# Optimization experiments

Measured on AMD Instinct MI355X. Metric: run time of the kernel, lower is better.

The kernel has to match this reference:

```python
import jax, jax.numpy as jnp
import numpy as np

B, T, K = 64, 4096, 48  # batch, seq_len, n_tags


def setup_inputs() -> dict:
    key = jax.random.key(0)
    k1, k2, k3 = jax.random.split(key, 3)
    labels = jax.random.randint(k1, (B, T), 0, K)
    y_true = jax.nn.one_hot(labels, K, dtype=jnp.float32)  # one-hot targets, per dense_loss docstring
    y_pred = jax.random.normal(k2, (B, T, K), dtype=jnp.float32)  # emission scores
    trans = jax.random.normal(k3, (K, K), dtype=jnp.float32) * 0.1  # transition matrix (glorot-ish scale)
    return {"y_true": y_true, "y_pred": y_pred, "trans": trans}


def reference(y_true, y_pred, trans):
    # mask: positions where all emission scores > -1e6 (padding marker)
    mask = jnp.all(y_pred > -1e6, axis=2, keepdims=True).astype(y_pred.dtype)  # (B,T,1)
    y_true = y_true * mask
    y_pred = y_pred * mask

    # target_score: per-label emission score + transition score of the true path
    point_score = jnp.einsum('bni,bni->b', y_true, y_pred)
    trans_score = jnp.einsum('bni,ij,bnj->b', y_true[:, :-1], trans, y_true[:, 1:])
    target = point_score + trans_score  # (B,)

    # log_norm_step recurrence (CRF forward algorithm), fused as a single scan
    init = y_pred[:, 0]  # (B,K)
    xs = jnp.swapaxes(y_pred[:, 1:], 0, 1)  # (T-1,B,K)
    ms = jnp.swapaxes(mask[:, 1:], 0, 1)    # (T-1,B,1)

    def step(s, xm):
        x, m = xm
        # logsumexp over previous-tag axis: s (B,K_prev) + trans (K_prev,K_cur)
        new = jax.scipy.special.logsumexp(s[:, :, None] + trans[None, :, :], axis=1) + x
        s = m * new + (1.0 - m) * s
        return s, None

    s_final, _ = jax.lax.scan(step, init, (xs, ms))
    log_norm = jax.scipy.special.logsumexp(s_final, axis=1)  # (B,)

    # dense_loss returns log_norm - target_score (negative log-likelihood per example)
    return log_norm - target
```

## Files before the change

### kernel.cpp

```cpp
#include <hip/hip_runtime.h>

#define BB 64
#define TT 4096
#define KK 48
#define UST 56
#define PST 56
#define WS_LS_OFF 16384
#define WS_U_OFF 32768
#define SEGBYTES 6144

typedef __bf16 bf16_t;
typedef bf16_t bf16x8 __attribute__((ext_vector_type(8)));
typedef float f32x4 __attribute__((ext_vector_type(4)));
typedef float f32x16 __attribute__((ext_vector_type(16)));

__device__ __forceinline__ float fexp(float x) {
    return __builtin_amdgcn_exp2f(x * 1.4426950408889634f);
}
__device__ __forceinline__ float flog2(float x) { return __builtin_amdgcn_logf(x); }
__device__ __forceinline__ float rdlanef(float v, int l) {
    return __int_as_float(__builtin_amdgcn_readlane(__float_as_int(v), l));
}
__device__ __forceinline__ unsigned int bf16bits(float f) {
    return (unsigned int)__builtin_bit_cast(unsigned short, (bf16_t)f);
}
__device__ __forceinline__ float bf2f(bf16_t h) {
    return __uint_as_float(((unsigned int)__builtin_bit_cast(unsigned short, h)) << 16);
}
__device__ __forceinline__ unsigned int pktrunc(float lo, float hi) {
    return __builtin_amdgcn_perm(__float_as_uint(hi), __float_as_uint(lo), 0x07060302u);
}

__global__ __launch_bounds__(256) void fused_kernel(
    const float* __restrict__ y_true, const float* __restrict__ y_pred,
    const float* __restrict__ trans, float* __restrict__ ws_target,
    int* __restrict__ ws_ls, bf16_t* __restrict__ ws_u, int nseg) {
    const int s = blockIdx.x, b = blockIdx.y;
    const int seglen = TT / nseg;
    const int nch = seglen / 64;
    const int tid = threadIdx.x;
    const int w = tid >> 6;
    const int lane = tid & 63;
    const int q = lane >> 4;
    const int n = lane & 15;
    const int ncol = 16 * w + n;

    __shared__ __align__(16) float4 exf[64 * 13];
    __shared__ __align__(16) bf16_t Ubuf[48 * UST + 16];
    __shared__ unsigned long long pb;
    __shared__ int lsb[4];

    bf16x8 afrag[3][2];
    if (w < 3) {
#pragma unroll
        for (int mt = 0; mt < 3; mt++) {
#pragma unroll
            for (int ks = 0; ks < 2; ks++) {
                bf16x8 f;
#pragma unroll
                for (int j = 0; j < 8; j++) {
                    int k = 32 * ks + 8 * q + j;
                    float v = (k < KK) ? fexp(trans[k * KK + 16 * mt + n]) : 0.0f;
                    f[j] = (bf16_t)v;
                }
                afrag[mt][ks] = f;
            }
        }
    }

    {
        uint4* p = (uint4*)Ubuf;
        for (int i = tid; i < (48 * UST + 16) / 8; i += 256) p[i] = make_uint4(0, 0, 0, 0);
    }
    __syncthreads();
    if (tid < KK) Ubuf[tid * UST + tid] = (bf16_t)1.0f;

    const bf16_t* bptr0 = &Ubuf[ncol * UST + 8 * q];
    const bf16_t* bptr1 = &Ubuf[ncol * UST + 32 + 8 * q];
    bf16_t* wp0 = &Ubuf[ncol * UST + 0 + 4 * q];
    bf16_t* wp1 = &Ubuf[ncol * UST + 16 + 4 * q];
    bf16_t* wp2 = &Ubuf[ncol * UST + 32 + 4 * q];

    f32x4 z4 = {0.0f, 0.0f, 0.0f, 0.0f};
    int ls = 0;
    int cnt = 0;
    float sc_acc = 0.0f;

    for (int ch = 0; ch < nch; ch++) {
        __syncthreads();
        if (w == 3) {
            const int t0c = s * seglen + ch * 64;
            const size_t rowbase = ((size_t)b * TT + t0c + lane) * KK;
            const float4* yp4 = (const float4*)(y_pred + rowbase);
            const float4* yt4 = (const float4*)(y_true + rowbase);
            float dot = 0.0f, labf = 0.0f, pmin = 1e30f;
            float4* exrow = &exf[lane * 13];
#pragma unroll 4
            for (int g = 0; g < 12; g++) {
                float4 p = yp4[g];
                float4 a = yt4[g];
                dot = fmaf(a.x, p.x, fmaf(a.y, p.y, fmaf(a.z, p.z, fmaf(a.w, p.w, dot))));
                float e0 = (float)(4 * g);
                labf = fmaf(a.x, e0, fmaf(a.y, e0 + 1.0f, fmaf(a.z, e0 + 2.0f, fmaf(a.w, e0 + 3.0f, labf))));
                pmin = fminf(pmin, fminf(fminf(p.x, p.y), fminf(p.z, p.w)));
                exrow[g] = make_float4(fexp(p.x), fexp(p.y), fexp(p.z), fexp(p.w));
            }
            bool mt_ok = pmin > -1e6f;
            unsigned long long bal = __ballot(mt_ok);
            if (lane == 0) pb = bal;

            float labB = 0.0f, pmB = 1e30f;
            const bool hasB = (t0c + 64 < TT);
            if (hasB && lane < 12) {
                const size_t bdbase = ((size_t)b * TT + t0c + 64) * KK;
                float4 a = ((const float4*)(y_true + bdbase))[lane];
                float4 p = ((const float4*)(y_pred + bdbase))[lane];
                float e0 = (float)(4 * lane);
                labB = fmaf(a.x, e0, fmaf(a.y, e0 + 1.0f, fmaf(a.z, e0 + 2.0f, a.w * (e0 + 3.0f))));
                pmB = fminf(fminf(p.x, p.y), fminf(p.z, p.w));
            }
#pragma unroll
            for (int off = 1; off < 16; off <<= 1) {
                labB += __shfl_xor(labB, off);
                pmB = fminf(pmB, __shfl_xor(pmB, off));
            }
            int labB_i = (int)(rdlanef(labB, 0) + 0.5f);
            float mB = (hasB && rdlanef(pmB, 0) > -1e6f) ? 1.0f : 0.0f;

            int labt = (int)(labf + 0.5f);
            float mft = mt_ok ? 1.0f : 0.0f;
            int lnx = __shfl(labt, (lane + 1) & 63);
            float mnx = __shfl(mft, (lane + 1) & 63);
            if (lane == 63) { lnx = labB_i; mnx = mB; }
            sc_acc += mft * dot + mft * mnx * trans[labt * KK + lnx];
        }
        __syncthreads();
        if (w < 3) {
            const unsigned long long mk = pb;
            const int tt0 = (s == 0 && ch == 0) ? 1 : 0;
            for (int tt = tt0; tt < 64; tt++) {
                if (!((mk >> tt) & 1ull)) continue;

                bf16x8 bf0 = __builtin_bit_cast(bf16x8, *(const uint4*)bptr0);
                bf16x8 bf1 = __builtin_bit_cast(bf16x8, *(const uint4*)bptr1);

                f32x4 acc0 = __builtin_amdgcn_mfma_f32_16x16x32_bf16(afrag[0][0], bf0, z4, 0, 0, 0);
                acc0 = __builtin_amdgcn_mfma_f32_16x16x32_bf16(afrag[0][1], bf1, acc0, 0, 0, 0);
                f32x4 acc1 = __builtin_amdgcn_mfma_f32_16x16x32_bf16(afrag[1][0], bf0, z4, 0, 0, 0);
                acc1 = __builtin_amdgcn_mfma_f32_16x16x32_bf16(afrag[1][1], bf1, acc1, 0, 0, 0);
                f32x4 acc2 = __builtin_amdgcn_mfma_f32_16x16x32_bf16(afrag[2][0], bf0, z4, 0, 0, 0);
                acc2 = __builtin_amdgcn_mfma_f32_16x16x32_bf16(afrag[2][1], bf1, acc2, 0, 0, 0);

                float4 ex0 = exf[tt * 13 + q];
                float4 ex1 = exf[tt * 13 + 4 + q];
                float4 ex2 = exf[tt * 13 + 8 + q];

                if (++cnt >= 6) {
                    float v00 = rdlanef(acc0[0], 0);
                    int k = (int)(__float_as_uint(v00) >> 23) - 127;
                    float r = __uint_as_float((unsigned int)(127 - k) << 23);
                    ls += k;
                    ex0.x *= r; ex0.y *= r; ex0.z *= r; ex0.w *= r;
                    ex1.x *= r; ex1.y *= r; ex1.z *= r; ex1.w *= r;
                    ex2.x *= r; ex2.y *= r; ex2.z *= r; ex2.w *= r;
                    cnt = 0;
                }

                *(uint2*)wp0 = make_uint2(pktrunc(acc0[0] * ex0.x, acc0[1] * ex0.y),
                                          pktrunc(acc0[2] * ex0.z, acc0[3] * ex0.w));
                *(uint2*)wp1 = make_uint2(pktrunc(acc1[0] * ex1.x, acc1[1] * ex1.y),
                                          pktrunc(acc1[2] * ex1.z, acc1[3] * ex1.w));
                *(uint2*)wp2 = make_uint2(pktrunc(acc2[0] * ex2.x, acc2[1] * ex2.y),
                                          pktrunc(acc2[2] * ex2.z, acc2[3] * ex2.w));
            }
        }
    }

    if (w == 3) {
#pragma unroll
        for (int off = 32; off; off >>= 1) sc_acc += __shfl_xor(sc_acc, off);
        if (lane == 0) ws_target[b * nseg + s] = sc_acc;
    }

    if (w < 3 && lane == 0) lsb[w] = ls;
    __syncthreads();
    if (w < 3 && lane < KK) {
        const int dl = ls - lsb[0];
        bf16_t* Uo = ws_u + (size_t)(b * nseg + s) * 3072;
        unsigned int wd[8];
#pragma unroll
        for (int j = 0; j < 8; j++) {
            float f0 = ldexpf(bf2f(Ubuf[(16 * w + 2 * j) * UST + lane]), dl);
            float f1 = ldexpf(bf2f(Ubuf[(16 * w + 2 * j + 1) * UST + lane]), dl);
            wd[j] = bf16bits(f0) | (bf16bits(f1) << 16);
        }
        *(uint4*)(Uo + (size_t)lane * 64 + 16 * w) = make_uint4(wd[0], wd[1], wd[2], wd[3]);
        *(uint4*)(Uo + (size_t)lane * 64 + 16 * w + 8) = make_uint4(wd[4], wd[5], wd[6], wd[7]);
    }
    if (tid == 0) ws_ls[b * nseg + s] = lsb[0];
}

__device__ __forceinline__ int chain_product(const bf16_t* __restrict__ A, bf16_t* Ub, int lane) {
    const int half = lane >> 5;
    const int l31 = lane & 31;
    f32x16 z16;
#pragma unroll
    for (int r = 0; r < 16; r++) z16[r] = 0.0f;

    bf16x8 af[2][3];
#pragma unroll
    for (int mt = 0; mt < 2; mt++) {
        int m = l31 + 32 * mt;
#pragma unroll
        for (int ks = 0; ks < 3; ks++) {
            if (m < KK)
                af[mt][ks] = __builtin_bit_cast(bf16x8, *(const uint4*)&A[(size_t)m * 64 + 16 * ks + 8 * half]);
            else
                af[mt][ks] = __builtin_bit_cast(bf16x8, make_uint4(0, 0, 0, 0));
        }
    }
    bf16x8 bg[3][2];
#pragma unroll
    for (int ks = 0; ks < 3; ks++)
#pragma unroll
        for (int nt = 0; nt < 2; nt++)
            bg[ks][nt] = __builtin_bit_cast(bf16x8, *(const uint4*)&Ub[(l31 + 32 * nt) * PST + 16 * ks + 8 * half]);

    f32x16 acc[4];
#pragma unroll
    for (int mt = 0; mt < 2; mt++)
#pragma unroll
        for (int nt = 0; nt < 2; nt++) {
            f32x16 a0 = __builtin_amdgcn_mfma_f32_32x32x16_bf16(af[mt][0], bg[0][nt], z16, 0, 0, 0);
            a0 = __builtin_amdgcn_mfma_f32_32x32x16_bf16(af[mt][1], bg[1][nt], a0, 0, 0, 0);
            acc[mt * 2 + nt] = __builtin_amdgcn_mfma_f32_32x32x16_bf16(af[mt][2], bg[2][nt], a0, 0, 0, 0);
        }

    float v00 = rdlanef(acc[0][0], 0);
    int k = (int)(__float_as_uint(v00) >> 23) - 127;
    float r = __uint_as_float((unsigned int)(127 - k) << 23);

#pragma unroll
    for (int mt = 0; mt < 2; mt++)
#pragma unroll
        for (int nt = 0; nt < 2; nt++) {
            int c = l31 + 32 * nt;
#pragma unroll
            for (int g = 0; g < 4; g++) {
                int a0 = 32 * mt + 8 * g + 4 * half;
                if (a0 < KK) {
                    const f32x16& Aq = acc[mt * 2 + nt];
                    unsigned int u0 = bf16bits(Aq[4 * g + 0] * r) | (bf16bits(Aq[4 * g + 1] * r) << 16);
                    unsigned int u1 = bf16bits(Aq[4 * g + 2] * r) | (bf16bits(Aq[4 * g + 3] * r) << 16);
                    *(uint2*)&Ub[c * PST + a0] = make_uint2(u0, u1);
                }
            }
        }
    return k;
}

__device__ __forceinline__ int chain_product_ldsA(const bf16_t* As, bf16_t* Ub, int lane) {
    const int half = lane >> 5;
    const int l31 = lane & 31;
    f32x16 z16;
#pragma unroll
    for (int r = 0; r < 16; r++) z16[r] = 0.0f;

    bf16x8 af[2][3];
#pragma unroll
    for (int mt = 0; mt < 2; mt++) {
        int m = l31 + 32 * mt;
#pragma unroll
        for (int ks = 0; ks < 3; ks++) {
            bf16x8 f;
#pragma unroll
            for (int j = 0; j < 8; j++) {
                int k = 16 * ks + 8 * half + j;
                f[j] = (m < KK) ? As[k * PST + m] : (bf16_t)0.0f;
            }
            af[mt][ks] = f;
        }
    }
    bf16x8 bg[3][2];
#pragma unroll
    for (int ks = 0; ks < 3; ks++)
#pragma unroll
        for (int nt = 0; nt < 2; nt++)
            bg[ks][nt] = __builtin_bit_cast(bf16x8, *(const uint4*)&Ub[(l31 + 32 * nt) * PST + 16 * ks + 8 * half]);

    f32x16 acc[4];
#pragma unroll
    for (int mt = 0; mt < 2; mt++)
#pragma unroll
        for (int nt = 0; nt < 2; nt++) {
            f32x16 a0 = __builtin_amdgcn_mfma_f32_32x32x16_bf16(af[mt][0], bg[0][nt], z16, 0, 0, 0);
            a0 = __builtin_amdgcn_mfma_f32_32x32x16_bf16(af[mt][1], bg[1][nt], a0, 0, 0, 0);
            acc[mt * 2 + nt] = __builtin_amdgcn_mfma_f32_32x32x16_bf16(af[mt][2], bg[2][nt], a0, 0, 0, 0);
        }

    float v00 = rdlanef(acc[0][0], 0);
    int k = (int)(__float_as_uint(v00) >> 23) - 127;
    float r = __uint_as_float((unsigned int)(127 - k) << 23);

#pragma unroll
    for (int mt = 0; mt < 2; mt++)
#pragma unroll
        for (int nt = 0; nt < 2; nt++) {
            int c = l31 + 32 * nt;
#pragma unroll
            for (int g = 0; g < 4; g++) {
                int a0 = 32 * mt + 8 * g + 4 * half;
                if (a0 < KK) {
                    const f32x16& Aq = acc[mt * 2 + nt];
                    unsigned int u0 = bf16bits(Aq[4 * g + 0] * r) | (bf16bits(Aq[4 * g + 1] * r) << 16);
                    unsigned int u1 = bf16bits(Aq[4 * g + 2] * r) | (bf16bits(Aq[4 * g + 3] * r) << 16);
                    *(uint2*)&Ub[c * PST + a0] = make_uint2(u0, u1);
                }
            }
        }
    return k;
}

__global__ __launch_bounds__(256) void fold8_kernel(
    bf16_t* __restrict__ ws_u, int* __restrict__ ws_ls, int nseg) {
    const int s8 = blockIdx.x, b = blockIdx.y;
    const int tid = threadIdx.x;
    const int w = tid >> 6, lane = tid & 63;
    const int base = b * nseg + s8 * 8;

    __shared__ __align__(16) bf16_t Ws[4][64 * PST];
    __shared__ int lsp[8];

    {
        const bf16_t* sE = ws_u + (size_t)(base + 2 * w) * 3072;
        for (int k = 0; k < KK; k++)
            Ws[w][lane * PST + k] = (lane < KK) ? sE[(size_t)k * 64 + lane] : (bf16_t)0.0f;
        int lsk = ws_ls[base + 2 * w] + ws_ls[base + 2 * w + 1];
        lsk += chain_product(ws_u + (size_t)(base + 2 * w + 1) * 3072, Ws[w], lane);
        if (lane == 0) lsp[w] = lsk;
    }
    __syncthreads();
    int k1 = 0;
    if (w == 0) k1 = chain_product_ldsA(Ws[1], Ws[0], lane);
    if (w == 2) {
        int k2 = chain_product_ldsA(Ws[3], Ws[2], lane);
        if (lane == 0) lsp[5] = k2;
    }
    __syncthreads();
    if (w == 0) {
        int k3 = chain_product_ldsA(Ws[2], Ws[0], lane);
        if (lane < KK) {
            bf16_t* Uo = ws_u + (size_t)base * 3072;
            unsigned int wd[24];
#pragma unroll
            for (int j = 0; j < 24; j++) {
                unsigned int lo = (unsigned int)__builtin_bit_cast(unsigned short, Ws[0][(2 * j) * PST + lane]);
                unsigned int hi = (unsigned int)__builtin_bit_cast(unsigned short, Ws[0][(2 * j + 1) * PST + lane]);
                wd[j] = lo | (hi << 16);
            }
#pragma unroll
            for (int g = 0; g < 6; g++)
                *(uint4*)(Uo + (size_t)lane * 64 + 8 * g) =
                    make_uint4(wd[4 * g], wd[4 * g + 1], wd[4 * g + 2], wd[4 * g + 3]);
        }
        if (lane == 0)
            ws_ls[base] = lsp[0] + lsp[1] + lsp[2] + lsp[3] + k1 + lsp[5] + k3;
    }
}

__global__ __launch_bounds__(256) void final_kernel(
    const float* __restrict__ y_pred, const bf16_t* __restrict__ ws_u,
    const int* __restrict__ ws_ls, const float* __restrict__ ws_target,
    float* __restrict__ out, int nseg) {
    const int b = blockIdx.x;
    const int tid = threadIdx.x;
    const int w = tid >> 6, lane = tid & 63;
    const int npart = nseg / 8;

    __shared__ __align__(16) bf16_t Ws[4][64 * PST];
    __shared__ int lsp[8];
    if (tid < 8) lsp[tid] = 0;
    __syncthreads();

    if (2 * w < npart) {
        const int slotE = b * nseg + 16 * w;
        const int slotL = slotE + 8;
        const bf16_t* sE = ws_u + (size_t)slotE * 3072;
        for (int k = 0; k < KK; k++)
            Ws[w][lane * PST + k] = (lane < KK) ? sE[(size_t)k * 64 + lane] : (bf16_t)0.0f;
        int lsk = ws_ls[slotE] + ws_ls[slotL];
        lsk += chain_product(ws_u + (size_t)slotL * 3072, Ws[w], lane);
        if (lane == 0) lsp[w] = lsk;
    }
    __syncthreads();
    int k1 = 0;
    if (npart >= 4 && w == 0) k1 = chain_product_ldsA(Ws[1], Ws[0], lane);
    if (npart == 8 && w == 2) {
        int k2 = chain_product_ldsA(Ws[3], Ws[2], lane);
        if (lane == 0) lsp[5] = k2;
    }
    __syncthreads();

    if (w == 0) {
        int k3 = 0;
        if (npart == 8) k3 = chain_product_ldsA(Ws[2], Ws[0], lane);
        float L = (float)(lsp[0] + lsp[1] + lsp[2] + lsp[3] + k1 + lsp[5] + k3);

        float x0 = (lane < KK) ? y_pred[(size_t)b * TT * KK + lane] : 0.0f;
        bool ok0 = (lane >= KK) || (x0 > -1e6f);
        bool m0 = (__ballot(ok0) == ~0ull);
        float xeff = (lane < KK) ? (m0 ? x0 : 0.0f) : 0.0f;
        float c0 = rdlanef(xeff, 0);
        float q0 = (lane < KK) ? fexp(xeff - c0) : 0.0f;

        float p = 0.0f;
        if (lane < KK) {
            for (int c = 0; c < KK; c++) {
                float qc = rdlanef(q0, c);
                p = fmaf(bf2f(Ws[0][c * PST + lane]), qc, p);
            }
        }
#pragma unroll
        for (int off = 32; off; off >>= 1) p += __shfl_xor(p, off);

        float tg = (lane < nseg) ? ws_target[b * nseg + lane] : 0.0f;
#pragma unroll
        for (int off = 32; off; off >>= 1) tg += __shfl_xor(tg, off);

        if (lane == 0) {
            out[b] = c0 + 0.6931471805599453f * (L + flog2(p)) - tg;
        }
    }
}

extern "C" void kernel_launch(void* const* d_in, const int* in_sizes, int n_in,
                              void* d_out, int out_size, void* d_ws, size_t ws_size,
                              hipStream_t stream) {
    const float* y_true = (const float*)d_in[0];
    const float* y_pred = (const float*)d_in[1];
    const float* trans = (const float*)d_in[2];
    float* out = (float*)d_out;

    int nseg = 16;
    if (ws_size >= (size_t)WS_U_OFF + (size_t)BB * 64 * SEGBYTES) nseg = 64;
    else if (ws_size >= (size_t)WS_U_OFF + (size_t)BB * 32 * SEGBYTES) nseg = 32;

    float* ws_target = (float*)d_ws;
    int* ws_ls = (int*)((char*)d_ws + WS_LS_OFF);
    bf16_t* ws_u = (bf16_t*)((char*)d_ws + WS_U_OFF);

    fused_kernel<<<dim3(nseg, BB), 256, 0, stream>>>(
        y_true, y_pred, trans, ws_target, ws_ls, ws_u, nseg);
    fold8_kernel<<<dim3(nseg / 8, BB), 256, 0, stream>>>(ws_u, ws_ls, nseg);
    final_kernel<<<BB, 256, 0, stream>>>(y_pred, ws_u, ws_ls, ws_target, out, nseg);
}
```

Baseline: 272.0 us.

## Keep recurrence state in registers via permlane swaps instead of LDS round-trip

The per-timestep state matrix U used to be written to shared memory as MFMA output and read back as the next MFMA B operand. It now stays in VGPRs, and v_permlane16_swap and v_permlane32_swap rearrange the accumulator layout into the B-fragment layout. The identity initialisation is built directly in registers, and LDS is written only once after the loop. Launch bounds also gain a min-blocks hint. This removes LDS store/load latency from the serial critical path, at the cost of extra permute instructions, selects and register pressure.

```diff
diff --git a/kernel.cpp b/kernel.cpp
--- a/kernel.cpp
+++ b/kernel.cpp
@@ -31,7 +31,7 @@
     return __builtin_amdgcn_perm(__float_as_uint(hi), __float_as_uint(lo), 0x07060302u);
 }
 
-__global__ __launch_bounds__(256) void fused_kernel(
+__global__ __launch_bounds__(256, 4) void fused_kernel(
     const float* __restrict__ y_true, const float* __restrict__ y_pred,
     const float* __restrict__ trans, float* __restrict__ ws_target,
     int* __restrict__ ws_ls, bf16_t* __restrict__ ws_u, int nseg) {
@@ -44,6 +44,7 @@
     const int q = lane >> 4;
     const int n = lane & 15;
     const int ncol = 16 * w + n;
+    const bool odd = (q & 1) != 0;
 
     __shared__ __align__(16) float4 exf[64 * 13];
     __shared__ __align__(16) bf16_t Ubuf[48 * UST + 16];
@@ -68,18 +69,14 @@
         }
     }
 
-    {
-        uint4* p = (uint4*)Ubuf;
-        for (int i = tid; i < (48 * UST + 16) / 8; i += 256) p[i] = make_uint4(0, 0, 0, 0);
-    }
-    __syncthreads();
-    if (tid < KK) Ubuf[tid * UST + tid] = (bf16_t)1.0f;
-
-    const bf16_t* bptr0 = &Ubuf[ncol * UST + 8 * q];
-    const bf16_t* bptr1 = &Ubuf[ncol * UST + 32 + 8 * q];
-    bf16_t* wp0 = &Ubuf[ncol * UST + 0 + 4 * q];
-    bf16_t* wp1 = &Ubuf[ncol * UST + 16 + 4 * q];
-    bf16_t* wp2 = &Ubuf[ncol * UST + 32 + 4 * q];
+    unsigned int u0[4], u1[4];
+#pragma unroll
+    for (int i = 0; i < 4; i++) {
+        int r0 = 8 * q + 2 * i;
+        u0[i] = ((r0 == ncol) ? 0x3F80u : 0u) | (((r0 + 1 == ncol) ? 0x3F80u : 0u) << 16);
+        int r1 = 32 + r0;
+        u1[i] = ((r1 == ncol) ? 0x3F80u : 0u) | (((r1 + 1 == ncol) ? 0x3F80u : 0u) << 16);
+    }
 
     f32x4 z4 = {0.0f, 0.0f, 0.0f, 0.0f};
     int ls = 0;
@@ -141,8 +138,8 @@
             for (int tt = tt0; tt < 64; tt++) {
                 if (!((mk >> tt) & 1ull)) continue;
 
-                bf16x8 bf0 = __builtin_bit_cast(bf16x8, *(const uint4*)bptr0);
-                bf16x8 bf1 = __builtin_bit_cast(bf16x8, *(const uint4*)bptr1);
+                bf16x8 bf0 = __builtin_bit_cast(bf16x8, make_uint4(u0[0], u0[1], u0[2], u0[3]));
+                bf16x8 bf1 = __builtin_bit_cast(bf16x8, make_uint4(u1[0], u1[1], u1[2], u1[3]));
 
                 f32x4 acc0 = __builtin_amdgcn_mfma_f32_16x16x32_bf16(afrag[0][0], bf0, z4, 0, 0, 0);
                 acc0 = __builtin_amdgcn_mfma_f32_16x16x32_bf16(afrag[0][1], bf1, acc0, 0, 0, 0);
@@ -160,20 +157,58 @@
                     int k = (int)(__float_as_uint(v00) >> 23) - 127;
                     float r = __uint_as_float((unsigned int)(127 - k) << 23);
                     ls += k;
+                    cnt = 0;
                     ex0.x *= r; ex0.y *= r; ex0.z *= r; ex0.w *= r;
                     ex1.x *= r; ex1.y *= r; ex1.z *= r; ex1.w *= r;
                     ex2.x *= r; ex2.y *= r; ex2.z *= r; ex2.w *= r;
-                    cnt = 0;
                 }
 
-                *(uint2*)wp0 = make_uint2(pktrunc(acc0[0] * ex0.x, acc0[1] * ex0.y),
-                                          pktrunc(acc0[2] * ex0.z, acc0[3] * ex0.w));
-                *(uint2*)wp1 = make_uint2(pktrunc(acc1[0] * ex1.x, acc1[1] * ex1.y),
-                                          pktrunc(acc1[2] * ex1.z, acc1[3] * ex1.w));
-                *(uint2*)wp2 = make_uint2(pktrunc(acc2[0] * ex2.x, acc2[1] * ex2.y),
-                                          pktrunc(acc2[2] * ex2.z, acc2[3] * ex2.w));
-            }
-        }
+                unsigned int m0a = pktrunc(acc0[0] * ex0.x, acc0[1] * ex0.y);
+                unsigned int m0b = pktrunc(acc0[2] * ex0.z, acc0[3] * ex0.w);
+                unsigned int m1a = pktrunc(acc1[0] * ex1.x, acc1[1] * ex1.y);
+                unsigned int m1b = pktrunc(acc1[2] * ex1.z, acc1[3] * ex1.w);
+                unsigned int m2a = pktrunc(acc2[0] * ex2.x, acc2[1] * ex2.y);
+                unsigned int m2b = pktrunc(acc2[2] * ex2.z, acc2[3] * ex2.w);
+
+                unsigned int X0 = m0a, X2 = m0a;
+                asm volatile("v_permlane16_swap_b32 %0, %1" : "+v"(X0), "+v"(X2));
+                unsigned int X1 = m0b, X3 = m0b;
+                asm volatile("v_permlane16_swap_b32 %0, %1" : "+v"(X1), "+v"(X3));
+                unsigned int Y0 = m1a, Y2 = m1a;
+                asm volatile("v_permlane16_swap_b32 %0, %1" : "+v"(Y0), "+v"(Y2));
+                unsigned int Y1 = m1b, Y3 = m1b;
+                asm volatile("v_permlane16_swap_b32 %0, %1" : "+v"(Y1), "+v"(Y3));
+                unsigned int Z0 = m2a, Z2 = m2a;
+                asm volatile("v_permlane16_swap_b32 %0, %1" : "+v"(Z0), "+v"(Z2));
+                unsigned int Z1 = m2b, Z3 = m2b;
+                asm volatile("v_permlane16_swap_b32 %0, %1" : "+v"(Z1), "+v"(Z3));
+
+                asm volatile("v_permlane32_swap_b32 %0, %1" : "+v"(X0), "+v"(Y0));
+                asm volatile("v_permlane32_swap_b32 %0, %1" : "+v"(X1), "+v"(Y1));
+                asm volatile("v_permlane32_swap_b32 %0, %1" : "+v"(X2), "+v"(Y2));
+                asm volatile("v_permlane32_swap_b32 %0, %1" : "+v"(X3), "+v"(Y3));
+                u0[0] = odd ? Y0 : X0;
+                u0[1] = odd ? Y1 : X1;
+                u0[2] = odd ? Y2 : X2;
+                u0[3] = odd ? Y3 : X3;
+
+                unsigned int W0 = Z0, W1 = Z1, W2 = Z2, W3 = Z3;
+                asm volatile("v_permlane32_swap_b32 %0, %1" : "+v"(Z0), "+v"(W0));
+                asm volatile("v_permlane32_swap_b32 %0, %1" : "+v"(Z1), "+v"(W1));
+                asm volatile("v_permlane32_swap_b32 %0, %1" : "+v"(Z2), "+v"(W2));
+                asm volatile("v_permlane32_swap_b32 %0, %1" : "+v"(Z3), "+v"(W3));
+                u1[0] = odd ? W0 : Z0;
+                u1[1] = odd ? W1 : Z1;
+                u1[2] = odd ? W2 : Z2;
+                u1[3] = odd ? W3 : Z3;
+            }
+        }
+    }
+
+    if (w < 3) {
+        *(uint4*)&Ubuf[ncol * UST + 8 * q] = make_uint4(u0[0], u0[1], u0[2], u0[3]);
+        if (q < 2)
+            *(uint4*)&Ubuf[ncol * UST + 32 + 8 * q] = make_uint4(u1[0], u1[1], u1[2], u1[3]);
     }
 
     if (w == 3) {
```

Result: slower. 286.1 us (+5.2%).
